# Optimization experiments

Measured on AMD Instinct MI355X. Metric: run time of the kernel, lower is better.

The kernel has to match this reference:

```python
import jax, jax.numpy as jnp
import numpy as np

NH, NKV, HD = 16, 4, 128
ROPE_THETA = 10000.0


def setup_inputs() -> dict:
    key = jax.random.key(0)
    ks = jax.random.split(key, 5)
    std = jnp.float32(0.02)
    return {
        "hidden_states": jax.random.normal(ks[0], (1, 2048, 2048), jnp.float32),
        "wq": jax.random.normal(ks[1], (2048, NH * HD), jnp.float32) * std,
        "wk": jax.random.normal(ks[2], (2048, NKV * HD), jnp.float32) * std,
        "wv": jax.random.normal(ks[3], (2048, NKV * HD), jnp.float32) * std,
        "wo": jax.random.normal(ks[4], (NH * HD, 2048), jnp.float32) * std,
    }


def _rope(x, cos, sin):
    # x: [B,S,n,hd]; pairs (even,odd) treated as complex, multiplied by cis(angle)
    xr = x.reshape(*x.shape[:-1], HD // 2, 2)
    re, im = xr[..., 0], xr[..., 1]
    c = cos[None, :, None, :]  # [1,S,1,hd/2]
    s = sin[None, :, None, :]
    out = jnp.stack((re * c - im * s, re * s + im * c), axis=-1)
    return out.reshape(x.shape)


def reference(hidden_states, wq, wk, wv, wo):
    B, S, H = hidden_states.shape
    q = (hidden_states @ wq).reshape(B, S, NH, HD)
    k = (hidden_states @ wk).reshape(B, S, NKV, HD)
    v = (hidden_states @ wv).reshape(B, S, NKV, HD)

    # precompute_freqs_cis (full rotary dim, rot_dim=None)
    freqs = 1.0 / (ROPE_THETA ** (jnp.arange(0, HD, 2, dtype=jnp.float32) / HD))
    ang = jnp.outer(jnp.arange(S, dtype=jnp.float32), freqs)  # [S, hd/2]
    cos, sin = jnp.cos(ang), jnp.sin(ang)

    q = _rope(q.astype(jnp.float32), cos, sin)
    k = _rope(k.astype(jnp.float32), cos, sin)

    # GQA: repeat_kv == repeat_interleave over head axis
    n_rep = NH // NKV
    k = jnp.repeat(k, n_rep, axis=2)  # [B,S,NH,HD]
    v = jnp.repeat(v, n_rep, axis=2)

    scale = jnp.float32(1.0 / np.sqrt(HD))
    scores = jnp.einsum("bqhd,bkhd->bhqk", q, k) * scale
    causal = jnp.tril(jnp.ones((S, S), dtype=bool))
    scores = jnp.where(causal[None, None], scores, jnp.float32(-1e9))
    attn = jax.nn.softmax(scores, axis=-1)
    out = jnp.einsum("bhqk,bkhd->bqhd", attn, v).reshape(B, S, NH * HD)
    return out @ wo
```

## Files before the change

### kernel.cpp

```cpp
#include <hip/hip_runtime.h>
#include <cstdint>

typedef __attribute__((ext_vector_type(8))) short short8;
typedef __attribute__((ext_vector_type(4))) float f32x4;

static __device__ __forceinline__ unsigned short f2bf(float x) {
  union { float f; unsigned int u; } c; c.f = x;
  unsigned int u = c.u;
  unsigned int r = (u + 0x7fffu + ((u >> 16) & 1u)) >> 16;
  return (unsigned short)r;
}

static __device__ __forceinline__ unsigned int cvt_pk_bf16(float a, float b) {
  unsigned int r;
  asm("v_cvt_pk_bf16_f32 %0, %1, %2" : "=v"(r) : "v"(a), "v"(b));
  return r;
}

static __device__ __forceinline__ void gl_lds16(const void* g, void* l) {
  __builtin_amdgcn_global_load_lds((const __attribute__((address_space(1))) void*)g,
                                   (__attribute__((address_space(3))) void*)l, 16, 0, 0);
}

__global__ __launch_bounds__(256) void k_sincos(float2* __restrict__ ctab) {
  int idx = blockIdx.x * 256 + threadIdx.x;
  int s = idx >> 6, i = idx & 63;
  float freq = powf(10000.0f, -(float)i / 64.0f);
  float sn, cs;
  sincosf((float)s * freq, &sn, &cs);
  ctab[idx] = make_float2(cs, sn);
}

__global__ __launch_bounds__(256) void k_f32_to_bf16(const float* __restrict__ src,
                                                     unsigned short* __restrict__ dst,
                                                     int n4) {
  int i = blockIdx.x * 256 + threadIdx.x;
  if (i >= n4) return;
  float4 v = reinterpret_cast<const float4*>(src)[i];
  ushort4 o;
  o.x = f2bf(v.x); o.y = f2bf(v.y); o.z = f2bf(v.z); o.w = f2bf(v.w);
  reinterpret_cast<ushort4*>(dst)[i] = o;
}

__global__ __launch_bounds__(256) void k_transpose_all(const float* __restrict__ wq,
                                                       const float* __restrict__ wk,
                                                       const float* __restrict__ wv,
                                                       const float* __restrict__ wo,
                                                       unsigned short* __restrict__ wqt,
                                                       unsigned short* __restrict__ wkt,
                                                       unsigned short* __restrict__ wvt,
                                                       unsigned short* __restrict__ wot) {
  __shared__ float tile[32][33];
  int id = blockIdx.x;
  const float* src; unsigned short* dst; int N, t;
  if (id < 4096)       { src = wq; dst = wqt; N = 2048; t = id; }
  else if (id < 8192)  { src = wo; dst = wot; N = 2048; t = id - 4096; }
  else if (id < 9216)  { src = wk; dst = wkt; N = 512;  t = id - 8192; }
  else                 { src = wv; dst = wvt; N = 512;  t = id - 9216; }
  const int K = 2048;
  int ntx = N >> 5;
  int bn = (t % ntx) * 32, bk = (t / ntx) * 32;
  int tx = threadIdx.x & 31, ty = threadIdx.x >> 5;
#pragma unroll
  for (int i = 0; i < 32; i += 8)
    tile[ty + i][tx] = src[(size_t)(bk + ty + i) * N + bn + tx];
  __syncthreads();
#pragma unroll
  for (int i = 0; i < 32; i += 8)
    dst[(size_t)(bn + ty + i) * K + bk + tx] = f2bf(tile[tx][ty + i]);
}

__global__ __launch_bounds__(256) void k_gemm_bf16(const unsigned short* __restrict__ A,
                                                   const unsigned short* __restrict__ Bt,
                                                   float* __restrict__ C,
                                                   unsigned short* __restrict__ Qd,
                                                   unsigned short* __restrict__ Kd,
                                                   unsigned short* __restrict__ VT,
                                                   const float2* __restrict__ ctab,
                                                   int M, int N, int K, int fuse) {
  __shared__ short sA[2][128 * 64];
  __shared__ short sB[2][64 * 64];
  int tid = threadIdx.x;
  int lane = tid & 63, wid = tid >> 6;
  int wr = wid >> 1, wc = wid & 1;

  int gx = gridDim.x, nwg = gx * gridDim.y;
  int flat = blockIdx.y * gx + blockIdx.x;
  int l = (flat & 7) * (nwg >> 3) + (flat >> 3);
  int bx = l % gx, by = l / gx;
  int m0 = by * 128, n0 = bx * 64;

  f32x4 acc[4][2] = {};

  int srcCol = (((tid & 7) ^ ((tid >> 3) & 7)) << 3);
  int rA = tid >> 3;
  const unsigned short* Ag = A + (size_t)(m0 + rA) * K + srcCol;
  const unsigned short* Bg = Bt + (size_t)(n0 + rA) * K + srcCol;
  int wb = (tid & ~63) * 8;

  int g = lane >> 4, fr = lane & 15, sw = fr & 7;

#define STAGE_G(buf, kof) do { \
    gl_lds16(Ag + (kof),                    &sA[buf][wb]); \
    gl_lds16(Ag + 32 * (size_t)K + (kof),   &sA[buf][2048 + wb]); \
    gl_lds16(Ag + 64 * (size_t)K + (kof),   &sA[buf][4096 + wb]); \
    gl_lds16(Ag + 96 * (size_t)K + (kof),   &sA[buf][6144 + wb]); \
    gl_lds16(Bg + (kof),                    &sB[buf][wb]); \
    gl_lds16(Bg + 32 * (size_t)K + (kof),   &sB[buf][2048 + wb]); \
  } while (0)

  int nt = K >> 6;
  STAGE_G(0, 0);
  __syncthreads();

  int cur = 0;
  for (int t = 0; t < nt; t++) {
    if (t + 1 < nt) STAGE_G(cur ^ 1, (size_t)((t + 1) << 6));
    const short* sAc = sA[cur];
    const short* sBc = sB[cur];
#pragma unroll
    for (int kk = 0; kk < 2; kk++) {
      int so = ((((kk << 2) + g) ^ sw) << 3);
      short8 af[4], bf2[2];
#pragma unroll
      for (int x = 0; x < 4; x++)
        af[x] = *(const short8*)(sAc + (wr * 64 + x * 16 + fr) * 64 + so);
#pragma unroll
      for (int ni = 0; ni < 2; ni++)
        bf2[ni] = *(const short8*)(sBc + (wc * 32 + ni * 16 + fr) * 64 + so);
#pragma unroll
      for (int x = 0; x < 4; x++)
#pragma unroll
        for (int ni = 0; ni < 2; ni++)
          acc[x][ni] = __builtin_amdgcn_mfma_f32_16x16x32_bf16(af[x], bf2[ni], acc[x][ni], 0, 0, 0);
    }
    __syncthreads();
    cur ^= 1;
  }
#undef STAGE_G

  int rb = m0 + wr * 64 + (g << 2);
  if (!fuse) {
#pragma unroll
    for (int ni = 0; ni < 2; ni++) {
      int col = n0 + wc * 32 + ni * 16 + fr;
#pragma unroll
      for (int x = 0; x < 4; x++)
#pragma unroll
        for (int j = 0; j < 4; j++)
          C[(size_t)(rb + x * 16 + j) * N + col] = acc[x][ni][j];
    }
    return;
  }

  const float QAMP = 0.12751742836257666f;
#pragma unroll
  for (int ni = 0; ni < 2; ni++) {
    int col = n0 + wc * 32 + ni * 16 + fr;
    if (col >= 2560) {
#pragma unroll
      for (int x = 0; x < 4; x++) {
        ushort4 pk;
        pk.x = f2bf(acc[x][ni][0]); pk.y = f2bf(acc[x][ni][1]);
        pk.z = f2bf(acc[x][ni][2]); pk.w = f2bf(acc[x][ni][3]);
        *(ushort4*)(VT + (size_t)(col - 2560) * 2048 + rb + x * 16) = pk;
      }
    } else {
      int ipair = (col & 127) >> 1;
      bool even = (col & 1) == 0;
      bool isQ = col < 2048;
      unsigned short* dst = isQ ? Qd : Kd;
      int stride = isQ ? 2048 : 512;
      int dcol = isQ ? col : (col - 2048);
      float amp = isQ ? QAMP : 1.0f;
#pragma unroll
      for (int x = 0; x < 4; x++) {
        f32x4 a = acc[x][ni];
        float p0 = __shfl_xor(a[0], 1), p1 = __shfl_xor(a[1], 1);
        float p2 = __shfl_xor(a[2], 1), p3 = __shfl_xor(a[3], 1);
        float pv[4] = {p0, p1, p2, p3};
#pragma unroll
        for (int j = 0; j < 4; j++) {
          int r = rb + x * 16 + j;
          float2 cs = ctab[r * 64 + ipair];
          float o = even ? (a[j] * cs.x - pv[j] * cs.y)
                         : (pv[j] * cs.y + a[j] * cs.x);
          dst[(size_t)r * stride + dcol] = f2bf(o * amp);
        }
      }
    }
  }
}

#define KSTR 136
#define VSTR 72
#define PSTR 72
__global__ __launch_bounds__(256) void k_attn_mfma(const unsigned short* __restrict__ Qb,
                                                   const unsigned short* __restrict__ Kb,
                                                   const unsigned short* __restrict__ Vt,
                                                   unsigned short* __restrict__ O) {
  __shared__ short sK[2][64 * KSTR];
  __shared__ short sV[2][128 * VSTR];
  __shared__ short sP[4][16 * PSTR];
  int h = blockIdx.y;
  int x = blockIdx.x;
  int qb = (h < 8) ? x : (31 - x);
  int q0 = qb * 64;
  int kvh = h >> 2;
  int tid = threadIdx.x, lane = tid & 63, w = tid >> 6;
  int fr = lane & 15, g = lane >> 4, kq = g << 3;

  short8 qf[4];
  {
    const unsigned short* qrow = Qb + (size_t)(q0 + w * 16 + fr) * 2048 + h * 128 + kq;
#pragma unroll
    for (int ko = 0; ko < 4; ko++) qf[ko] = *(const short8*)(qrow + ko * 32);
  }

  f32x4 oacc[8];
#pragma unroll
  for (int nd = 0; nd < 8; nd++) oacc[nd] = (f32x4){0.f, 0.f, 0.f, 0.f};
  float m_i = -3e38f;
  float l_i = 0.f;

  int skr = tid >> 2, skc = (tid & 3) << 5;
  int svd = tid >> 1, svc = (tid & 1) << 5;
  const unsigned short* Kbase = Kb + (size_t)kvh * 128 + skc;
  const unsigned short* Vbase = Vt + (size_t)(kvh * 128 + svd) * 2048 + svc;
  short* pw = (short*)sP[w];
  int kdOff = skr * KSTR + skc;
  int vdOff = svd * VSTR + svc;

  short8 kreg[4], vreg[4];
  {
    const short8* ks = (const short8*)(Kbase + (size_t)skr * 512);
    const short8* vs = (const short8*)(Vbase);
#pragma unroll
    for (int j = 0; j < 4; j++) { kreg[j] = ks[j]; vreg[j] = vs[j]; }
  }
  {
    short* kd = sK[0] + kdOff; short* vd = sV[0] + vdOff;
#pragma unroll
    for (int j = 0; j < 4; j++) { *(short8*)(kd + j * 8) = kreg[j]; *(short8*)(vd + j * 8) = vreg[j]; }
  }
  if (qb >= 1) {
    const short8* ks = (const short8*)(Kbase + (size_t)(64 + skr) * 512);
    const short8* vs = (const short8*)(Vbase + 64);
#pragma unroll
    for (int j = 0; j < 4; j++) { kreg[j] = ks[j]; vreg[j] = vs[j]; }
  }
  __syncthreads();

  int qrowS = q0 + w * 16 + fr;

  for (int kt = 0; kt <= qb; kt++) {
    int c = kt & 1;
    const short* sKc = sK[c];
    const short* sVc = sV[c];

    f32x4 sacc[4];
#pragma unroll
    for (int ni = 0; ni < 4; ni++) sacc[ni] = (f32x4){0.f, 0.f, 0.f, 0.f};
    __builtin_amdgcn_s_setprio(1);
#pragma unroll
    for (int ko = 0; ko < 4; ko++)
#pragma unroll
      for (int ni = 0; ni < 4; ni++) {
        short8 kf = *(const short8*)(sKc + (ni * 16 + fr) * KSTR + kq + ko * 32);
        sacc[ni] = __builtin_amdgcn_mfma_f32_16x16x32_bf16(kf, qf[ko], sacc[ni], 0, 0, 0);
      }
    __builtin_amdgcn_s_setprio(0);

    if (kt == qb) {
      int k0 = kt * 64;
#pragma unroll
      for (int ni = 0; ni < 4; ni++) {
        int kc = k0 + ni * 16 + (g << 2);
#pragma unroll
        for (int j = 0; j < 4; j++)
          if (kc + j > qrowS) sacc[ni][j] = -3e38f;
      }
    }

    float t0 = fmaxf(fmaxf(sacc[0][0], sacc[0][1]), fmaxf(sacc[0][2], sacc[0][3]));
    float t1 = fmaxf(fmaxf(sacc[1][0], sacc[1][1]), fmaxf(sacc[1][2], sacc[1][3]));
    float t2 = fmaxf(fmaxf(sacc[2][0], sacc[2][1]), fmaxf(sacc[2][2], sacc[2][3]));
    float t3 = fmaxf(fmaxf(sacc[3][0], sacc[3][1]), fmaxf(sacc[3][2], sacc[3][3]));
    float tm = fmaxf(fmaxf(t0, t1), fmaxf(t2, t3));
    tm = fmaxf(tm, __shfl_xor(tm, 16));
    tm = fmaxf(tm, __shfl_xor(tm, 32));

    if (!__all(tm <= m_i + 8.0f)) {
      float mn = fmaxf(m_i, tm);
      float sc = exp2f(m_i - mn);
      m_i = mn;
      float scj[4];
#pragma unroll
      for (int j = 0; j < 4; j++) scj[j] = __shfl(sc, (g << 2) + j);
#pragma unroll
      for (int nd = 0; nd < 8; nd++)
#pragma unroll
        for (int j = 0; j < 4; j++) oacc[nd][j] *= scj[j];
      l_i *= sc;
    }

    float ps = 0.f;
#pragma unroll
    for (int ni = 0; ni < 4; ni++) {
      float p0 = exp2f(sacc[ni][0] - m_i);
      float p1 = exp2f(sacc[ni][1] - m_i);
      float p2 = exp2f(sacc[ni][2] - m_i);
      float p3 = exp2f(sacc[ni][3] - m_i);
      ps += (p0 + p1) + (p2 + p3);
      uint2 pk;
      pk.x = cvt_pk_bf16(p0, p1);
      pk.y = cvt_pk_bf16(p2, p3);
      *(uint2*)(pw + fr * PSTR + ni * 16 + (g << 2)) = pk;
    }
    ps += __shfl_xor(ps, 16);
    ps += __shfl_xor(ps, 32);
    l_i += ps;

    __builtin_amdgcn_s_setprio(1);
#pragma unroll
    for (int ks = 0; ks < 2; ks++) {
      short8 pa = *(const short8*)(pw + fr * PSTR + kq + ks * 32);
#pragma unroll
      for (int nd = 0; nd < 8; nd++) {
        short8 vb = *(const short8*)(sVc + (nd * 16 + fr) * VSTR + kq + ks * 32);
        oacc[nd] = __builtin_amdgcn_mfma_f32_16x16x32_bf16(pa, vb, oacc[nd], 0, 0, 0);
      }
    }
    __builtin_amdgcn_s_setprio(0);

    if (kt < qb) {
      short* kd = sK[c ^ 1] + kdOff; short* vd = sV[c ^ 1] + vdOff;
#pragma unroll
      for (int j = 0; j < 4; j++) { *(short8*)(kd + j * 8) = kreg[j]; *(short8*)(vd + j * 8) = vreg[j]; }
      if (kt + 1 < qb) {
        int k2 = (kt + 2) * 64;
        const short8* ks = (const short8*)(Kbase + (size_t)(k2 + skr) * 512);
        const short8* vs = (const short8*)(Vbase + k2);
#pragma unroll
        for (int j = 0; j < 4; j++) { kreg[j] = ks[j]; vreg[j] = vs[j]; }
      }
      __syncthreads();
    }
  }

  int orow = q0 + w * 16 + (g << 2);
#pragma unroll
  for (int j = 0; j < 4; j++) {
    float lj = __shfl(l_i, (g << 2) + j);
    float inv = 1.0f / lj;
#pragma unroll
    for (int nd = 0; nd < 8; nd++)
      O[(size_t)(orow + j) * 2048 + h * 128 + nd * 16 + fr] = f2bf(oacc[nd][j] * inv);
  }
}

extern "C" void kernel_launch(void* const* d_in, const int* in_sizes, int n_in,
                              void* d_out, int out_size, void* d_ws, size_t ws_size,
                              hipStream_t stream) {
  const float* hs = (const float*)d_in[0];
  const float* wq = (const float*)d_in[1];
  const float* wk = (const float*)d_in[2];
  const float* wv = (const float*)d_in[3];
  const float* wo = (const float*)d_in[4];
  char* ws = (char*)d_ws;

  unsigned short* hb   = (unsigned short*)(ws);
  unsigned short* wqt  = (unsigned short*)(ws + 8388608);
  unsigned short* wkt  = (unsigned short*)(ws + 16777216);
  unsigned short* wvt  = (unsigned short*)(ws + 18874368);
  unsigned short* wot  = (unsigned short*)(ws + 20971520);
  unsigned short* q_bf = (unsigned short*)(ws + 29360128);
  unsigned short* k_bf = (unsigned short*)(ws + 37748736);
  unsigned short* vt_bf= (unsigned short*)(ws + 39845888);
  float2* ctab         = (float2*)(ws + 41943040);
  unsigned short* ao   = hb;
  float* out = (float*)d_out;

  k_sincos<<<512, 256, 0, stream>>>(ctab);
  k_f32_to_bf16<<<4096, 256, 0, stream>>>(hs, hb, 2048 * 2048 / 4);
  k_transpose_all<<<10240, 256, 0, stream>>>(wq, wk, wv, wo, wqt, wkt, wvt, wot);

  k_gemm_bf16<<<dim3(48, 16), 256, 0, stream>>>(hb, wqt, (float*)nullptr,
                                                q_bf, k_bf, vt_bf, ctab,
                                                2048, 3072, 2048, 1);

  k_attn_mfma<<<dim3(32, 16), 256, 0, stream>>>(q_bf, k_bf, vt_bf, ao);

  k_gemm_bf16<<<dim3(32, 16), 256, 0, stream>>>(ao, wot, out,
                                                (unsigned short*)nullptr,
                                                (unsigned short*)nullptr,
                                                (unsigned short*)nullptr,
                                                (const float2*)nullptr,
                                                2048, 2048, 2048, 0);
}
```

Measured before the change: 143.6 us.

## Split attention KV loop across two wave groups and merge prep kernels

Attention blocks grow to 512 threads: two groups of four waves each process alternate KV tiles for the same 64 query rows. They keep separate online-softmax states that are merged through LDS at the end. Blocks are reordered so the longest causal query blocks launch first. The three prep kernels (sincos table, hidden-state bf16 cast, weight transposes) are merged into one launch to cut launch overhead. In exchange the attention kernel adds extra syncs per iteration, LDS traffic for the merge, and more register pressure per block.

```diff
diff --git a/kernel.cpp b/kernel.cpp
--- a/kernel.cpp
+++ b/kernel.cpp
@@ -22,36 +22,36 @@
                                    (__attribute__((address_space(3))) void*)l, 16, 0, 0);
 }
 
-__global__ __launch_bounds__(256) void k_sincos(float2* __restrict__ ctab) {
-  int idx = blockIdx.x * 256 + threadIdx.x;
-  int s = idx >> 6, i = idx & 63;
-  float freq = powf(10000.0f, -(float)i / 64.0f);
-  float sn, cs;
-  sincosf((float)s * freq, &sn, &cs);
-  ctab[idx] = make_float2(cs, sn);
-}
-
-__global__ __launch_bounds__(256) void k_f32_to_bf16(const float* __restrict__ src,
-                                                     unsigned short* __restrict__ dst,
-                                                     int n4) {
-  int i = blockIdx.x * 256 + threadIdx.x;
-  if (i >= n4) return;
-  float4 v = reinterpret_cast<const float4*>(src)[i];
-  ushort4 o;
-  o.x = f2bf(v.x); o.y = f2bf(v.y); o.z = f2bf(v.z); o.w = f2bf(v.w);
-  reinterpret_cast<ushort4*>(dst)[i] = o;
-}
-
-__global__ __launch_bounds__(256) void k_transpose_all(const float* __restrict__ wq,
-                                                       const float* __restrict__ wk,
-                                                       const float* __restrict__ wv,
-                                                       const float* __restrict__ wo,
-                                                       unsigned short* __restrict__ wqt,
-                                                       unsigned short* __restrict__ wkt,
-                                                       unsigned short* __restrict__ wvt,
-                                                       unsigned short* __restrict__ wot) {
+__global__ __launch_bounds__(256) void k_prep(const float* __restrict__ wq,
+                                              const float* __restrict__ wk,
+                                              const float* __restrict__ wv,
+                                              const float* __restrict__ wo,
+                                              const float* __restrict__ hs,
+                                              unsigned short* __restrict__ wqt,
+                                              unsigned short* __restrict__ wkt,
+                                              unsigned short* __restrict__ wvt,
+                                              unsigned short* __restrict__ wot,
+                                              unsigned short* __restrict__ hb,
+                                              float2* __restrict__ ctab) {
+  int id = blockIdx.x;
+  if (id >= 10240) {
+    if (id < 14336) {
+      int i = (id - 10240) * 256 + threadIdx.x;
+      float4 v = reinterpret_cast<const float4*>(hs)[i];
+      ushort4 o;
+      o.x = f2bf(v.x); o.y = f2bf(v.y); o.z = f2bf(v.z); o.w = f2bf(v.w);
+      reinterpret_cast<ushort4*>(hb)[i] = o;
+    } else {
+      int idx = (id - 14336) * 256 + threadIdx.x;
+      int s = idx >> 6, i = idx & 63;
+      float freq = powf(10000.0f, -(float)i / 64.0f);
+      float sn, cs;
+      sincosf((float)s * freq, &sn, &cs);
+      ctab[idx] = make_float2(cs, sn);
+    }
+    return;
+  }
   __shared__ float tile[32][33];
-  int id = blockIdx.x;
   const float* src; unsigned short* dst; int N, t;
   if (id < 4096)       { src = wq; dst = wqt; N = 2048; t = id; }
   else if (id < 8192)  { src = wo; dst = wot; N = 2048; t = id - 4096; }
@@ -195,24 +195,26 @@
 #define KSTR 136
 #define VSTR 72
 #define PSTR 72
-__global__ __launch_bounds__(256) void k_attn_mfma(const unsigned short* __restrict__ Qb,
+__global__ __launch_bounds__(512) void k_attn_mfma(const unsigned short* __restrict__ Qb,
                                                    const unsigned short* __restrict__ Kb,
                                                    const unsigned short* __restrict__ Vt,
                                                    unsigned short* __restrict__ O) {
   __shared__ short sK[2][64 * KSTR];
   __shared__ short sV[2][128 * VSTR];
-  __shared__ short sP[4][16 * PSTR];
-  int h = blockIdx.y;
-  int x = blockIdx.x;
-  int qb = (h < 8) ? x : (31 - x);
+  __shared__ short sP[8][16 * PSTR];
+  int b = blockIdx.x;
+  int qb = 31 - (b >> 4);
+  int h = b & 15;
   int q0 = qb * 64;
   int kvh = h >> 2;
-  int tid = threadIdx.x, lane = tid & 63, w = tid >> 6;
+  int tid = threadIdx.x, lane = tid & 63, w8 = tid >> 6;
+  int g4 = w8 & 3;
+  int p = w8 >> 2;
   int fr = lane & 15, g = lane >> 4, kq = g << 3;
 
   short8 qf[4];
   {
-    const unsigned short* qrow = Qb + (size_t)(q0 + w * 16 + fr) * 2048 + h * 128 + kq;
+    const unsigned short* qrow = Qb + (size_t)(q0 + g4 * 16 + fr) * 2048 + h * 128 + kq;
 #pragma unroll
     for (int ko = 0; ko < 4; ko++) qf[ko] = *(const short8*)(qrow + ko * 32);
   }
@@ -223,139 +225,174 @@
   float m_i = -3e38f;
   float l_i = 0.f;
 
-  int skr = tid >> 2, skc = (tid & 3) << 5;
-  int svd = tid >> 1, svc = (tid & 1) << 5;
+  int half = tid >> 8;
+  int t2 = tid & 255;
+  int skr = t2 >> 2, skc = (t2 & 3) << 5;
+  int svd = t2 >> 1, svc = (t2 & 1) << 5;
   const unsigned short* Kbase = Kb + (size_t)kvh * 128 + skc;
   const unsigned short* Vbase = Vt + (size_t)(kvh * 128 + svd) * 2048 + svc;
-  short* pw = (short*)sP[w];
+  short* pw = (short*)sP[w8];
   int kdOff = skr * KSTR + skc;
   int vdOff = svd * VSTR + svc;
 
   short8 kreg[4], vreg[4];
-  {
-    const short8* ks = (const short8*)(Kbase + (size_t)skr * 512);
-    const short8* vs = (const short8*)(Vbase);
+  if (half <= qb) {
+    const short8* ks = (const short8*)(Kbase + (size_t)(half * 64 + skr) * 512);
+    const short8* vs = (const short8*)(Vbase + half * 64);
 #pragma unroll
     for (int j = 0; j < 4; j++) { kreg[j] = ks[j]; vreg[j] = vs[j]; }
-  }
-  {
-    short* kd = sK[0] + kdOff; short* vd = sV[0] + vdOff;
+    short* kd = sK[half] + kdOff; short* vd = sV[half] + vdOff;
 #pragma unroll
     for (int j = 0; j < 4; j++) { *(short8*)(kd + j * 8) = kreg[j]; *(short8*)(vd + j * 8) = vreg[j]; }
   }
-  if (qb >= 1) {
-    const short8* ks = (const short8*)(Kbase + (size_t)(64 + skr) * 512);
-    const short8* vs = (const short8*)(Vbase + 64);
+  if (2 + half <= qb) {
+    const short8* ks = (const short8*)(Kbase + (size_t)((2 + half) * 64 + skr) * 512);
+    const short8* vs = (const short8*)(Vbase + (2 + half) * 64);
 #pragma unroll
     for (int j = 0; j < 4; j++) { kreg[j] = ks[j]; vreg[j] = vs[j]; }
   }
   __syncthreads();
 
-  int qrowS = q0 + w * 16 + fr;
-
-  for (int kt = 0; kt <= qb; kt++) {
-    int c = kt & 1;
-    const short* sKc = sK[c];
-    const short* sVc = sV[c];
-
-    f32x4 sacc[4];
-#pragma unroll
-    for (int ni = 0; ni < 4; ni++) sacc[ni] = (f32x4){0.f, 0.f, 0.f, 0.f};
-    __builtin_amdgcn_s_setprio(1);
-#pragma unroll
-    for (int ko = 0; ko < 4; ko++)
+  int qrowS = q0 + g4 * 16 + fr;
+  int nIter = (qb + 2) >> 1;
+
+  for (int i = 0; i < nIter; i++) {
+    int t = 2 * i + p;
+    if (t <= qb) {
+      const short* sKc = sK[p];
+      const short* sVc = sV[p];
+
+      f32x4 sacc[4];
+#pragma unroll
+      for (int ni = 0; ni < 4; ni++) sacc[ni] = (f32x4){0.f, 0.f, 0.f, 0.f};
+      __builtin_amdgcn_s_setprio(1);
+#pragma unroll
+      for (int ko = 0; ko < 4; ko++)
+#pragma unroll
+        for (int ni = 0; ni < 4; ni++) {
+          short8 kf = *(const short8*)(sKc + (ni * 16 + fr) * KSTR + kq + ko * 32);
+          sacc[ni] = __builtin_amdgcn_mfma_f32_16x16x32_bf16(kf, qf[ko], sacc[ni], 0, 0, 0);
+        }
+      __builtin_amdgcn_s_setprio(0);
+
+      if (t == qb) {
+        int k0 = t * 64;
+#pragma unroll
+        for (int ni = 0; ni < 4; ni++) {
+          int kc = k0 + ni * 16 + (g << 2);
+#pragma unroll
+          for (int j = 0; j < 4; j++)
+            if (kc + j > qrowS) sacc[ni][j] = -3e38f;
+        }
+      }
+
+      float t0m = fmaxf(fmaxf(sacc[0][0], sacc[0][1]), fmaxf(sacc[0][2], sacc[0][3]));
+      float t1m = fmaxf(fmaxf(sacc[1][0], sacc[1][1]), fmaxf(sacc[1][2], sacc[1][3]));
+      float t2m = fmaxf(fmaxf(sacc[2][0], sacc[2][1]), fmaxf(sacc[2][2], sacc[2][3]));
+      float t3m = fmaxf(fmaxf(sacc[3][0], sacc[3][1]), fmaxf(sacc[3][2], sacc[3][3]));
+      float tm = fmaxf(fmaxf(t0m, t1m), fmaxf(t2m, t3m));
+      tm = fmaxf(tm, __shfl_xor(tm, 16));
+      tm = fmaxf(tm, __shfl_xor(tm, 32));
+
+      if (!__all(tm <= m_i + 8.0f)) {
+        float mn = fmaxf(m_i, tm);
+        float sc = exp2f(m_i - mn);
+        m_i = mn;
+        float scj[4];
+#pragma unroll
+        for (int j = 0; j < 4; j++) scj[j] = __shfl(sc, (g << 2) + j);
+#pragma unroll
+        for (int nd = 0; nd < 8; nd++)
+#pragma unroll
+          for (int j = 0; j < 4; j++) oacc[nd][j] *= scj[j];
+        l_i *= sc;
+      }
+
+      float ps = 0.f;
 #pragma unroll
       for (int ni = 0; ni < 4; ni++) {
-        short8 kf = *(const short8*)(sKc + (ni * 16 + fr) * KSTR + kq + ko * 32);
-        sacc[ni] = __builtin_amdgcn_mfma_f32_16x16x32_bf16(kf, qf[ko], sacc[ni], 0, 0, 0);
-      }
-    __builtin_amdgcn_s_setprio(0);
-
-    if (kt == qb) {
-      int k0 = kt * 64;
-#pragma unroll
-      for (int ni = 0; ni < 4; ni++) {
-        int kc = k0 + ni * 16 + (g << 2);
-#pragma unroll
-        for (int j = 0; j < 4; j++)
-          if (kc + j > qrowS) sacc[ni][j] = -3e38f;
-      }
-    }
-
-    float t0 = fmaxf(fmaxf(sacc[0][0], sacc[0][1]), fmaxf(sacc[0][2], sacc[0][3]));
-    float t1 = fmaxf(fmaxf(sacc[1][0], sacc[1][1]), fmaxf(sacc[1][2], sacc[1][3]));
-    float t2 = fmaxf(fmaxf(sacc[2][0], sacc[2][1]), fmaxf(sacc[2][2], sacc[2][3]));
-    float t3 = fmaxf(fmaxf(sacc[3][0], sacc[3][1]), fmaxf(sacc[3][2], sacc[3][3]));
-    float tm = fmaxf(fmaxf(t0, t1), fmaxf(t2, t3));
-    tm = fmaxf(tm, __shfl_xor(tm, 16));
-    tm = fmaxf(tm, __shfl_xor(tm, 32));
-
-    if (!__all(tm <= m_i + 8.0f)) {
-      float mn = fmaxf(m_i, tm);
-      float sc = exp2f(m_i - mn);
-      m_i = mn;
-      float scj[4];
-#pragma unroll
-      for (int j = 0; j < 4; j++) scj[j] = __shfl(sc, (g << 2) + j);
+        float p0 = exp2f(sacc[ni][0] - m_i);
+        float p1 = exp2f(sacc[ni][1] - m_i);
+        float p2 = exp2f(sacc[ni][2] - m_i);
+        float p3 = exp2f(sacc[ni][3] - m_i);
+        ps += (p0 + p1) + (p2 + p3);
+        uint2 pk;
+        pk.x = cvt_pk_bf16(p0, p1);
+        pk.y = cvt_pk_bf16(p2, p3);
+        *(uint2*)(pw + fr * PSTR + ni * 16 + (g << 2)) = pk;
+      }
+      ps += __shfl_xor(ps, 16);
+      ps += __shfl_xor(ps, 32);
+      l_i += ps;
+
+      __builtin_amdgcn_s_setprio(1);
+#pragma unroll
+      for (int ks = 0; ks < 2; ks++) {
+        short8 pa = *(const short8*)(pw + fr * PSTR + kq + ks * 32);
+#pragma unroll
+        for (int nd = 0; nd < 8; nd++) {
+          short8 vb = *(const short8*)(sVc + (nd * 16 + fr) * VSTR + kq + ks * 32);
+          oacc[nd] = __builtin_amdgcn_mfma_f32_16x16x32_bf16(pa, vb, oacc[nd], 0, 0, 0);
+        }
+      }
+      __builtin_amdgcn_s_setprio(0);
+    }
+
+    if (i + 1 < nIter) {
+      __syncthreads();
+      int tn = 2 * (i + 1) + half;
+      if (tn <= qb) {
+        short* kd = sK[half] + kdOff; short* vd = sV[half] + vdOff;
+#pragma unroll
+        for (int j = 0; j < 4; j++) { *(short8*)(kd + j * 8) = kreg[j]; *(short8*)(vd + j * 8) = vreg[j]; }
+      }
+      int tl = 2 * (i + 2) + half;
+      if (tl <= qb) {
+        const short8* ks = (const short8*)(Kbase + (size_t)(tl * 64 + skr) * 512);
+        const short8* vs = (const short8*)(Vbase + tl * 64);
+#pragma unroll
+        for (int j = 0; j < 4; j++) { kreg[j] = ks[j]; vreg[j] = vs[j]; }
+      }
+      __syncthreads();
+    }
+  }
+
+  __syncthreads();
+  float* onum = (float*)sK;
+  float* mlb = (float*)sV;
+  if (p == 1) {
+    int r0 = g4 * 16;
+#pragma unroll
+    for (int j = 0; j < 4; j++)
 #pragma unroll
       for (int nd = 0; nd < 8; nd++)
-#pragma unroll
-        for (int j = 0; j < 4; j++) oacc[nd][j] *= scj[j];
-      l_i *= sc;
-    }
-
-    float ps = 0.f;
-#pragma unroll
-    for (int ni = 0; ni < 4; ni++) {
-      float p0 = exp2f(sacc[ni][0] - m_i);
-      float p1 = exp2f(sacc[ni][1] - m_i);
-      float p2 = exp2f(sacc[ni][2] - m_i);
-      float p3 = exp2f(sacc[ni][3] - m_i);
-      ps += (p0 + p1) + (p2 + p3);
-      uint2 pk;
-      pk.x = cvt_pk_bf16(p0, p1);
-      pk.y = cvt_pk_bf16(p2, p3);
-      *(uint2*)(pw + fr * PSTR + ni * 16 + (g << 2)) = pk;
-    }
-    ps += __shfl_xor(ps, 16);
-    ps += __shfl_xor(ps, 32);
-    l_i += ps;
-
-    __builtin_amdgcn_s_setprio(1);
-#pragma unroll
-    for (int ks = 0; ks < 2; ks++) {
-      short8 pa = *(const short8*)(pw + fr * PSTR + kq + ks * 32);
+        onum[(r0 + (g << 2) + j) * 128 + nd * 16 + fr] = oacc[nd][j];
+    if (g == 0) {
+      mlb[(r0 + fr) * 2] = m_i;
+      mlb[(r0 + fr) * 2 + 1] = l_i;
+    }
+  }
+  __syncthreads();
+  if (p == 0) {
+    int orow = q0 + g4 * 16 + (g << 2);
+    int r0 = g4 * 16;
+#pragma unroll
+    for (int j = 0; j < 4; j++) {
+      int rl = (g << 2) + j;
+      float ma = __shfl(m_i, rl);
+      float la = __shfl(l_i, rl);
+      float mb = mlb[(r0 + rl) * 2];
+      float lb = mlb[(r0 + rl) * 2 + 1];
+      float M = fmaxf(ma, mb);
+      float wa = exp2f(ma - M), wbv = exp2f(mb - M);
+      float inv = 1.0f / (wa * la + wbv * lb);
 #pragma unroll
       for (int nd = 0; nd < 8; nd++) {
-        short8 vb = *(const short8*)(sVc + (nd * 16 + fr) * VSTR + kq + ks * 32);
-        oacc[nd] = __builtin_amdgcn_mfma_f32_16x16x32_bf16(pa, vb, oacc[nd], 0, 0, 0);
-      }
-    }
-    __builtin_amdgcn_s_setprio(0);
-
-    if (kt < qb) {
-      short* kd = sK[c ^ 1] + kdOff; short* vd = sV[c ^ 1] + vdOff;
-#pragma unroll
-      for (int j = 0; j < 4; j++) { *(short8*)(kd + j * 8) = kreg[j]; *(short8*)(vd + j * 8) = vreg[j]; }
-      if (kt + 1 < qb) {
-        int k2 = (kt + 2) * 64;
-        const short8* ks = (const short8*)(Kbase + (size_t)(k2 + skr) * 512);
-        const short8* vs = (const short8*)(Vbase + k2);
-#pragma unroll
-        for (int j = 0; j < 4; j++) { kreg[j] = ks[j]; vreg[j] = vs[j]; }
-      }
-      __syncthreads();
-    }
-  }
-
-  int orow = q0 + w * 16 + (g << 2);
-#pragma unroll
-  for (int j = 0; j < 4; j++) {
-    float lj = __shfl(l_i, (g << 2) + j);
-    float inv = 1.0f / lj;
-#pragma unroll
-    for (int nd = 0; nd < 8; nd++)
-      O[(size_t)(orow + j) * 2048 + h * 128 + nd * 16 + fr] = f2bf(oacc[nd][j] * inv);
+        float ob = onum[(r0 + rl) * 128 + nd * 16 + fr];
+        O[(size_t)(orow + j) * 2048 + h * 128 + nd * 16 + fr] =
+            f2bf((wa * oacc[nd][j] + wbv * ob) * inv);
+      }
+    }
   }
 }
 
@@ -381,15 +418,13 @@
   unsigned short* ao   = hb;
   float* out = (float*)d_out;
 
-  k_sincos<<<512, 256, 0, stream>>>(ctab);
-  k_f32_to_bf16<<<4096, 256, 0, stream>>>(hs, hb, 2048 * 2048 / 4);
-  k_transpose_all<<<10240, 256, 0, stream>>>(wq, wk, wv, wo, wqt, wkt, wvt, wot);
+  k_prep<<<14848, 256, 0, stream>>>(wq, wk, wv, wo, hs, wqt, wkt, wvt, wot, hb, ctab);
 
   k_gemm_bf16<<<dim3(48, 16), 256, 0, stream>>>(hb, wqt, (float*)nullptr,
                                                 q_bf, k_bf, vt_bf, ctab,
                                                 2048, 3072, 2048, 1);
 
-  k_attn_mfma<<<dim3(32, 16), 256, 0, stream>>>(q_bf, k_bf, vt_bf, ao);
+  k_attn_mfma<<<512, 512, 0, stream>>>(q_bf, k_bf, vt_bf, ao);
 
   k_gemm_bf16<<<dim3(32, 16), 256, 0, stream>>>(ao, wot, out,
                                                 (unsigned short*)nullptr,
```

Result: faster. 136.6 us (-4.9%).
